# Performance work log

Hardware: AMD Instinct MI355X
Metric: run time of the kernel (lower is better)

The kernel has to match this reference:

```python
import jax, jax.numpy as jnp
import numpy as np
import math

N_EMBD = 1024
N_HEAD = 16
HEAD_DIM = N_EMBD // N_HEAD

def setup_inputs() -> dict:
    key = jax.random.key(0)
    k1, k2, k3, k4, k5 = jax.random.split(key, 5)
    s = 1.0 / math.sqrt(N_EMBD)
    x = jax.random.normal(k1, (4, 2048, N_EMBD), dtype=jnp.float32)
    W_qkv = jax.random.normal(k2, (N_EMBD, 3 * N_EMBD), dtype=jnp.float32) * s
    b_qkv = jnp.zeros((3 * N_EMBD,), dtype=jnp.float32)
    W_proj = jax.random.normal(k3, (N_EMBD, N_EMBD), dtype=jnp.float32) * s
    b_proj = jnp.zeros((N_EMBD,), dtype=jnp.float32)
    return {"x": x, "W_qkv": W_qkv, "b_qkv": b_qkv, "W_proj": W_proj, "b_proj": b_proj}

def reference(x, W_qkv, b_qkv, W_proj, b_proj):
    B, T, C = x.shape
    H, D = N_HEAD, HEAD_DIM
    qkv = x @ W_qkv + b_qkv                      # (B,T,3C)
    qkv = qkv.reshape(B, T, 3, H, D)
    q = jnp.transpose(qkv[:, :, 0], (0, 2, 1, 3))  # (B,H,T,D)
    k = jnp.transpose(qkv[:, :, 1], (0, 2, 1, 3))
    v = jnp.transpose(qkv[:, :, 2], (0, 2, 1, 3))
    scale = 1.0 / math.sqrt(D)
    att = jnp.einsum('bhtd,bhsd->bhts', q, k) * scale  # (B,H,T,T)
    causal = jnp.tril(jnp.ones((T, T), dtype=bool))
    att = jnp.where(causal[None, None], att, -jnp.inf)
    att = jax.nn.softmax(att, axis=-1)
    out = jnp.einsum('bhts,bhsd->bhtd', att, v)   # (B,H,T,D)
    out = jnp.transpose(out, (0, 2, 1, 3)).reshape(B, T, C)
    return out @ W_proj + b_proj
```

## Files before the change

kernel.cpp:

```cpp
#include <hip/hip_runtime.h>
#include <stdint.h>


typedef __attribute__((ext_vector_type(8))) __bf16 bf16x8_t;
typedef __attribute__((ext_vector_type(4))) float f32x4_t;
typedef __attribute__((ext_vector_type(16))) float f32x16_t;
typedef __attribute__((ext_vector_type(4))) unsigned short u16x4_t;
typedef __attribute__((ext_vector_type(4))) unsigned int u32x4_t;

static __device__ __forceinline__ unsigned short f2bf(float f) {
  union { float f; unsigned u; } c; c.f = f;
  unsigned r = c.u + 0x7FFFu + ((c.u >> 16) & 1u);
  return (unsigned short)(r >> 16);
}

static __device__ __forceinline__ unsigned cvt_pk_bf16(float lo, float hi) {
  unsigned r;
  asm volatile("v_cvt_pk_bf16_f32 %0, %1, %2" : "=v"(r) : "v"(lo), "v"(hi));
  return r;
}

static __device__ __forceinline__ void perm32swap(unsigned& a, unsigned& b) {
  asm volatile("v_permlane32_swap_b32 %0, %1" : "+v"(a), "+v"(b));
}

static __device__ __forceinline__ f32x16_t zero16() {
  f32x16_t v;
#pragma unroll
  for (int i = 0; i < 16; ++i) v[i] = 0.f;
  return v;
}

static __device__ __forceinline__ void gload16(const void* g, void* lds) {
  __builtin_amdgcn_global_load_lds(
      (const __attribute__((address_space(1))) unsigned int*)g,
      (__attribute__((address_space(3))) unsigned int*)(uint32_t)(uintptr_t)lds,
      16, 0, 0);
}

__global__ __launch_bounds__(256) void k_cast_bf16(const float* __restrict__ in,
                                                   unsigned short* __restrict__ out) {
  int i = blockIdx.x * 256 + threadIdx.x;
  float4 v = ((const float4*)in)[i];
  u16x4_t r = { f2bf(v.x), f2bf(v.y), f2bf(v.z), f2bf(v.w) };
  ((u16x4_t*)out)[i] = r;
}

__global__ __launch_bounds__(256) void k_transpose_cast(const float* __restrict__ W,
                                                        unsigned short* __restrict__ Wt,
                                                        int Kd, int Nd) {
  __shared__ float tile[32][33];
  int n0 = blockIdx.x * 32, k0 = blockIdx.y * 32;
  int tx = threadIdx.x, ty = threadIdx.y;
#pragma unroll
  for (int i = 0; i < 4; ++i)
    tile[ty + 8 * i][tx] = W[(size_t)(k0 + ty + 8 * i) * Nd + n0 + tx];
  __syncthreads();
#pragma unroll
  for (int i = 0; i < 4; ++i)
    Wt[(size_t)(n0 + ty + 8 * i) * Kd + k0 + tx] = f2bf(tile[tx][ty + 8 * i]);
}

static __device__ __forceinline__ void gemm_core(
    const unsigned short* __restrict__ A, const unsigned short* __restrict__ Bt,
    int Kd, int bm0, int bn0,
    unsigned short (*As)[8192], unsigned short (*Bs)[8192],
    f32x4_t acc[8][4]) {
  const int tid = threadIdx.x;
  const int lane = tid & 63;
  const int wid = tid >> 6;
  const int wm = wid >> 2, wn = wid & 3;
  const int l15 = lane & 15, lhi = (lane >> 4) & 3;
  const int r0 = tid >> 2;
  const int cd = tid & 3;
  const int NK = Kd >> 6;

  auto STAGE = [&](int kt, int h, int sl) {
#pragma unroll
    for (int j = 0; j < 2; ++j) {
      const int row = r0 + 128 * j;
      const int sc = cd ^ ((row >> 1) & 3);
      gload16(A + (size_t)(bm0 + row) * Kd + kt * 64 + h * 32 + sc * 8,
              &As[sl * 2 + h][row * 32 + cd * 8]);
    }
#pragma unroll
    for (int j = 0; j < 2; ++j) {
      const int row = r0 + 128 * j;
      const int sc = cd ^ ((row >> 1) & 3);
      gload16(Bt + (size_t)(bn0 + row) * Kd + kt * 64 + h * 32 + sc * 8,
              &Bs[sl * 2 + h][row * 32 + cd * 8]);
    }
  };

  STAGE(0, 0, 0);
  STAGE(0, 1, 0);
  for (int kt = 0; kt < NK; ++kt) {
    const int sl = kt & 1;
    const int ktn = (kt + 1 < NK) ? kt + 1 : kt;
#pragma unroll
    for (int h = 0; h < 2; ++h) {
      asm volatile("s_waitcnt vmcnt(4)" ::: "memory");
      __builtin_amdgcn_sched_barrier(0);
      __builtin_amdgcn_s_barrier();
      __builtin_amdgcn_sched_barrier(0);
      STAGE(ktn, h, sl ^ 1);
      bf16x8_t af[8], bfr[4];
#pragma unroll
      for (int m = 0; m < 8; ++m) {
        const int ar = wm * 128 + m * 16 + l15;
        af[m] = *(const bf16x8_t*)&As[sl * 2 + h][ar * 32 + ((lhi ^ ((ar >> 1) & 3)) << 3)];
      }
#pragma unroll
      for (int n = 0; n < 4; ++n) {
        const int br = wn * 64 + n * 16 + l15;
        bfr[n] = *(const bf16x8_t*)&Bs[sl * 2 + h][br * 32 + ((lhi ^ ((br >> 1) & 3)) << 3)];
      }
      __builtin_amdgcn_s_setprio(1);
#pragma unroll
      for (int m = 0; m < 8; ++m)
#pragma unroll
        for (int n = 0; n < 4; ++n)
          acc[m][n] = __builtin_amdgcn_mfma_f32_16x16x32_bf16(af[m], bfr[n], acc[m][n], 0, 0, 0);
      __builtin_amdgcn_s_setprio(0);
    }
  }
}

__global__ __launch_bounds__(512, 2) void k_gemm_qkv(
    const unsigned short* __restrict__ A, const unsigned short* __restrict__ Bt,
    const float* __restrict__ bias,
    unsigned short* __restrict__ Qo, unsigned short* __restrict__ Ko,
    unsigned short* __restrict__ Vo) {
  __shared__ alignas(16) unsigned short As[4][8192];
  __shared__ alignas(16) unsigned short Bs[4][8192];
  const int orig = blockIdx.x;
  const int swz = (orig & 7) * 48 + (orig >> 3);
  const int by = swz / 12, bx = swz % 12;
  f32x4_t acc[8][4];
  f32x4_t z = {0.f, 0.f, 0.f, 0.f};
#pragma unroll
  for (int m = 0; m < 8; ++m)
#pragma unroll
    for (int n = 0; n < 4; ++n) acc[m][n] = z;
  gemm_core(A, Bt, 1024, by * 256, bx * 256, As, Bs, acc);
  const int tid = threadIdx.x, lane = tid & 63;
  const int wid = tid >> 6, wm = wid >> 2, wn = wid & 3;
  const int l15 = lane & 15, lhi = (lane >> 4) & 3;
#pragma unroll
  for (int n = 0; n < 4; ++n) {
    int col = bx * 256 + wn * 64 + n * 16 + l15;
    int which = col >> 10;
    int h = (col >> 6) & 15;
    int d = col & 63;
    float bv = bias[col];
#pragma unroll
    for (int m = 0; m < 8; ++m)
#pragma unroll
      for (int r = 0; r < 4; ++r) {
        int row = by * 256 + wm * 128 + m * 16 + lhi * 4 + r;
        int b = row >> 11, t = row & 2047;
        float val = acc[m][n][r] + bv;
        if (which == 0)
          Qo[(size_t)((b * 16 + h) * 2048 + t) * 64 + d] = f2bf(val * 0.18033688011112042f);
        else if (which == 1)
          Ko[(size_t)((b * 16 + h) * 2048 + t) * 64 + d] = f2bf(val);
        else
          Vo[(size_t)((b * 16 + h) * 64 + d) * 2048 + t] = f2bf(val);
      }
  }
}

__global__ __launch_bounds__(512, 2) void k_gemm_proj(
    const unsigned short* __restrict__ A, const unsigned short* __restrict__ Bt,
    const float* __restrict__ bias, float* __restrict__ out) {
  __shared__ alignas(16) unsigned short As[4][8192];
  __shared__ alignas(16) unsigned short Bs[4][8192];
  const int orig = blockIdx.x;
  const int swz = (orig & 7) * 16 + (orig >> 3);
  const int by = swz >> 2, bx = swz & 3;
  f32x4_t acc[8][4];
  f32x4_t z = {0.f, 0.f, 0.f, 0.f};
#pragma unroll
  for (int m = 0; m < 8; ++m)
#pragma unroll
    for (int n = 0; n < 4; ++n) acc[m][n] = z;
  gemm_core(A, Bt, 1024, by * 256, bx * 256, As, Bs, acc);
  const int tid = threadIdx.x, lane = tid & 63;
  const int wid = tid >> 6, wm = wid >> 2, wn = wid & 3;
  const int l15 = lane & 15, lhi = (lane >> 4) & 3;
#pragma unroll
  for (int n = 0; n < 4; ++n) {
    int col = bx * 256 + wn * 64 + n * 16 + l15;
    float bv = bias[col];
#pragma unroll
    for (int m = 0; m < 8; ++m)
#pragma unroll
      for (int r = 0; r < 4; ++r) {
        int row = by * 256 + wm * 128 + m * 16 + lhi * 4 + r;
        out[(size_t)row * 1024 + col] = acc[m][n][r] + bv;
      }
  }
}

__global__ __launch_bounds__(256) void k_attn(const unsigned short* __restrict__ Q,
                                              const unsigned short* __restrict__ K,
                                              const unsigned short* __restrict__ Vt,
                                              unsigned short* __restrict__ O) {
  __shared__ alignas(16) unsigned short KT[2][4096];
  __shared__ alignas(16) unsigned short VT[2][4096];
  const int flat = blockIdx.x;
  const int bx = 15 - (flat >> 6);
  const int bh = flat & 63;
  const int tid = threadIdx.x;
  const int lane = tid & 63;
  const int w = tid >> 6;
  const int l31 = lane & 31;
  const int hi = lane >> 5;
  const int sw = l31 & 7;
  const unsigned short* Qh = Q + (size_t)bh * 2048 * 64;
  const unsigned short* Kh = K + (size_t)bh * 2048 * 64;
  const unsigned short* Vh = Vt + (size_t)bh * 64 * 2048;
  const int qrow = bx * 128 + w * 32;
  const int qg = qrow + l31;
  const int NT = 2 * bx + 2;

  bf16x8_t qf[4];
#pragma unroll
  for (int s = 0; s < 4; ++s)
    qf[s] = *(const bf16x8_t*)&Qh[(size_t)qg * 64 + s * 16 + hi * 8];

  f32x16_t ot0 = zero16(), ot1 = zero16();
  float m_r = -1e30f, l_r = 0.f;

  const int srow = tid >> 3;
  const int ssw = 8 * ((tid & 7) ^ (srow & 7));
  auto STAGE = [&](int t_, int buf_) {
#pragma unroll
    for (int i = 0; i < 2; ++i) {
      const int r_ = i * 32 + srow;
      gload16(Kh + (size_t)(t_ * 64 + r_) * 64 + ssw, &KT[buf_][i * 2048 + tid * 8]);
      gload16(Vh + (size_t)r_ * 2048 + t_ * 64 + ssw, &VT[buf_][i * 2048 + tid * 8]);
    }
  };

  STAGE(0, 0);
  __syncthreads();
  for (int t = 0; t < NT; ++t) {
    const int buf = t & 1;
    if (t + 1 < NT) STAGE(t + 1, buf ^ 1);
    if (t * 64 <= qrow + 31) {
      f32x16_t st[2];
#pragma unroll
      for (int tt = 0; tt < 2; ++tt) {
        st[tt] = zero16();
        const unsigned short* kr = &KT[buf][(tt * 32 + l31) * 64];
#pragma unroll
        for (int s = 0; s < 4; ++s) {
          bf16x8_t kf = *(const bf16x8_t*)&kr[((2 * s + hi) ^ sw) * 8];
          st[tt] = __builtin_amdgcn_mfma_f32_32x32x16_bf16(kf, qf[s], st[tt], 0, 0, 0);
        }
      }
      if (t * 64 + 63 > qrow) {
#pragma unroll
        for (int tt = 0; tt < 2; ++tt)
#pragma unroll
          for (int r = 0; r < 16; ++r) {
            int kv = t * 64 + tt * 32 + (r & 3) + 8 * (r >> 2) + 4 * hi;
            if (kv > qg) st[tt][r] = -1e30f;
          }
      }
      float mx = st[0][0];
#pragma unroll
      for (int tt = 0; tt < 2; ++tt)
#pragma unroll
        for (int r = 0; r < 16; ++r) mx = fmaxf(mx, st[tt][r]);
      mx = fmaxf(mx, __shfl_xor(mx, 32));
      float mnew = fmaxf(m_r, mx);
      float resc = __builtin_amdgcn_exp2f(m_r - mnew);
      float u = 0.f;
#pragma unroll
      for (int tt = 0; tt < 2; ++tt)
#pragma unroll
        for (int r = 0; r < 16; ++r) {
          float pv = __builtin_amdgcn_exp2f(st[tt][r] - mnew);
          st[tt][r] = pv;
          u += pv;
        }
      u += __shfl_xor(u, 32);
      l_r = l_r * resc + u;
      m_r = mnew;
      ot0 *= resc;
      ot1 *= resc;
#pragma unroll
      for (int tt = 0; tt < 2; ++tt) {
        unsigned W0 = cvt_pk_bf16(st[tt][0], st[tt][1]);
        unsigned W1 = cvt_pk_bf16(st[tt][2], st[tt][3]);
        unsigned W2 = cvt_pk_bf16(st[tt][4], st[tt][5]);
        unsigned W3 = cvt_pk_bf16(st[tt][6], st[tt][7]);
        unsigned W4 = cvt_pk_bf16(st[tt][8], st[tt][9]);
        unsigned W5 = cvt_pk_bf16(st[tt][10], st[tt][11]);
        unsigned W6 = cvt_pk_bf16(st[tt][12], st[tt][13]);
        unsigned W7 = cvt_pk_bf16(st[tt][14], st[tt][15]);
        perm32swap(W0, W2);
        perm32swap(W1, W3);
        perm32swap(W4, W6);
        perm32swap(W5, W7);
        u32x4_t fe = {W0, W1, W2, W3};
        u32x4_t fo = {W4, W5, W6, W7};
        bf16x8_t pe = __builtin_bit_cast(bf16x8_t, fe);
        bf16x8_t po = __builtin_bit_cast(bf16x8_t, fo);
        const unsigned short* vr0 = &VT[buf][l31 * 64];
        const unsigned short* vr1 = &VT[buf][(32 + l31) * 64];
        bf16x8_t ve0 = *(const bf16x8_t*)&vr0[((4 * tt + hi) ^ sw) * 8];
        bf16x8_t vo0 = *(const bf16x8_t*)&vr0[((4 * tt + 2 + hi) ^ sw) * 8];
        bf16x8_t ve1 = *(const bf16x8_t*)&vr1[((4 * tt + hi) ^ sw) * 8];
        bf16x8_t vo1 = *(const bf16x8_t*)&vr1[((4 * tt + 2 + hi) ^ sw) * 8];
        ot0 = __builtin_amdgcn_mfma_f32_32x32x16_bf16(ve0, pe, ot0, 0, 0, 0);
        ot0 = __builtin_amdgcn_mfma_f32_32x32x16_bf16(vo0, po, ot0, 0, 0, 0);
        ot1 = __builtin_amdgcn_mfma_f32_32x32x16_bf16(ve1, pe, ot1, 0, 0, 0);
        ot1 = __builtin_amdgcn_mfma_f32_32x32x16_bf16(vo1, po, ot1, 0, 0, 0);
      }
    }
    __syncthreads();
  }
  const float inv = 1.0f / l_r;
  const int b = bh >> 4, h = bh & 15;
  unsigned short* orow = O + (size_t)(b * 2048 + qg) * 1024 + h * 64;
#pragma unroll
  for (int m = 0; m < 4; ++m) {
    u16x4_t r0, r1;
#pragma unroll
    for (int j = 0; j < 4; ++j) {
      r0[j] = f2bf(ot0[4 * m + j] * inv);
      r1[j] = f2bf(ot1[4 * m + j] * inv);
    }
    *(u16x4_t*)&orow[8 * m + 4 * hi] = r0;
    *(u16x4_t*)&orow[32 + 8 * m + 4 * hi] = r1;
  }
}

extern "C" void kernel_launch(void* const* d_in, const int* in_sizes, int n_in,
                              void* d_out, int out_size, void* d_ws, size_t ws_size,
                              hipStream_t stream) {
  const float* x     = (const float*)d_in[0];
  const float* Wqkv  = (const float*)d_in[1];
  const float* bqkv  = (const float*)d_in[2];
  const float* Wproj = (const float*)d_in[3];
  const float* bproj = (const float*)d_in[4];
  float* out = (float*)d_out;

  char* ws = (char*)d_ws;
  unsigned short* xb     = (unsigned short*)(ws);
  unsigned short* wqkvT  = (unsigned short*)(ws + 16777216);
  unsigned short* wprojT = (unsigned short*)(ws + 23068672);
  unsigned short* Qb     = (unsigned short*)(ws + 25165824);
  unsigned short* Kb     = (unsigned short*)(ws + 41943040);
  unsigned short* Vb     = (unsigned short*)(ws + 58720256);
  unsigned short* Ob     = (unsigned short*)(ws + 75497472);

  k_cast_bf16<<<8192, 256, 0, stream>>>(x, xb);
  k_transpose_cast<<<dim3(96, 32), dim3(32, 8), 0, stream>>>(Wqkv, wqkvT, 1024, 3072);
  k_transpose_cast<<<dim3(32, 32), dim3(32, 8), 0, stream>>>(Wproj, wprojT, 1024, 1024);
  k_gemm_qkv<<<384, 512, 0, stream>>>(xb, wqkvT, bqkv, Qb, Kb, Vb);
  k_attn<<<1024, 256, 0, stream>>>(Qb, Kb, Vb, Ob);
  k_gemm_proj<<<128, 512, 0, stream>>>(Ob, wprojT, bproj, out);
}
```

Before: 290.9 us.

## Stage V-tile transpose through LDS and remap GEMM block-to-XCD tiling

The QKV GEMM epilogue for V columns now writes the bf16 tile into a swizzled shared buffer, then emits 16-byte coalesced stores along t into the transposed V layout, replacing scattered 2-byte strided stores. Shared memory is merged into one flat buffer so the epilogue can reuse it. Block index mapping for both GEMMs is changed so each XCD gets a 2D rectangle of tiles, aiming to improve L2 reuse of A and B panels. This adds two block barriers and an LDS round trip for the V blocks.

```diff
diff --git a/kernel.cpp b/kernel.cpp
--- a/kernel.cpp
+++ b/kernel.cpp
@@ -63,9 +63,7 @@
 
 static __device__ __forceinline__ void gemm_core(
     const unsigned short* __restrict__ A, const unsigned short* __restrict__ Bt,
-    int Kd, int bm0, int bn0,
-    unsigned short (*As)[8192], unsigned short (*Bs)[8192],
-    f32x4_t acc[8][4]) {
+    int Kd, int bm0, int bn0, unsigned short* SH, f32x4_t acc[8][4]) {
   const int tid = threadIdx.x;
   const int lane = tid & 63;
   const int wid = tid >> 6;
@@ -76,19 +74,21 @@
   const int NK = Kd >> 6;
 
   auto STAGE = [&](int kt, int h, int sl) {
+    unsigned short* Asl = SH + (sl * 2 + h) * 8192;
+    unsigned short* Bsl = SH + 32768 + (sl * 2 + h) * 8192;
 #pragma unroll
     for (int j = 0; j < 2; ++j) {
       const int row = r0 + 128 * j;
       const int sc = cd ^ ((row >> 1) & 3);
       gload16(A + (size_t)(bm0 + row) * Kd + kt * 64 + h * 32 + sc * 8,
-              &As[sl * 2 + h][row * 32 + cd * 8]);
+              &Asl[row * 32 + cd * 8]);
     }
 #pragma unroll
     for (int j = 0; j < 2; ++j) {
       const int row = r0 + 128 * j;
       const int sc = cd ^ ((row >> 1) & 3);
       gload16(Bt + (size_t)(bn0 + row) * Kd + kt * 64 + h * 32 + sc * 8,
-              &Bs[sl * 2 + h][row * 32 + cd * 8]);
+              &Bsl[row * 32 + cd * 8]);
     }
   };
 
@@ -104,16 +104,18 @@
       __builtin_amdgcn_s_barrier();
       __builtin_amdgcn_sched_barrier(0);
       STAGE(ktn, h, sl ^ 1);
+      const unsigned short* Asl = SH + (sl * 2 + h) * 8192;
+      const unsigned short* Bsl = SH + 32768 + (sl * 2 + h) * 8192;
       bf16x8_t af[8], bfr[4];
 #pragma unroll
       for (int m = 0; m < 8; ++m) {
         const int ar = wm * 128 + m * 16 + l15;
-        af[m] = *(const bf16x8_t*)&As[sl * 2 + h][ar * 32 + ((lhi ^ ((ar >> 1) & 3)) << 3)];
+        af[m] = *(const bf16x8_t*)&Asl[ar * 32 + ((lhi ^ ((ar >> 1) & 3)) << 3)];
       }
 #pragma unroll
       for (int n = 0; n < 4; ++n) {
         const int br = wn * 64 + n * 16 + l15;
-        bfr[n] = *(const bf16x8_t*)&Bs[sl * 2 + h][br * 32 + ((lhi ^ ((br >> 1) & 3)) << 3)];
+        bfr[n] = *(const bf16x8_t*)&Bsl[br * 32 + ((lhi ^ ((br >> 1) & 3)) << 3)];
       }
       __builtin_amdgcn_s_setprio(1);
 #pragma unroll
@@ -131,60 +133,88 @@
     const float* __restrict__ bias,
     unsigned short* __restrict__ Qo, unsigned short* __restrict__ Ko,
     unsigned short* __restrict__ Vo) {
-  __shared__ alignas(16) unsigned short As[4][8192];
-  __shared__ alignas(16) unsigned short Bs[4][8192];
+  __shared__ alignas(16) unsigned short SH[65536];
   const int orig = blockIdx.x;
-  const int swz = (orig & 7) * 48 + (orig >> 3);
-  const int by = swz / 12, bx = swz % 12;
+  const int xcd = orig & 7, lc = orig >> 3;
+  const int by = (xcd >> 1) * 8 + lc / 6;
+  const int bx = (xcd & 1) * 6 + lc % 6;
   f32x4_t acc[8][4];
   f32x4_t z = {0.f, 0.f, 0.f, 0.f};
 #pragma unroll
   for (int m = 0; m < 8; ++m)
 #pragma unroll
     for (int n = 0; n < 4; ++n) acc[m][n] = z;
-  gemm_core(A, Bt, 1024, by * 256, bx * 256, As, Bs, acc);
+  gemm_core(A, Bt, 1024, by * 256, bx * 256, SH, acc);
   const int tid = threadIdx.x, lane = tid & 63;
   const int wid = tid >> 6, wm = wid >> 2, wn = wid & 3;
   const int l15 = lane & 15, lhi = (lane >> 4) & 3;
-#pragma unroll
-  for (int n = 0; n < 4; ++n) {
-    int col = bx * 256 + wn * 64 + n * 16 + l15;
-    int which = col >> 10;
-    int h = (col >> 6) & 15;
-    int d = col & 63;
-    float bv = bias[col];
-#pragma unroll
-    for (int m = 0; m < 8; ++m)
-#pragma unroll
-      for (int r = 0; r < 4; ++r) {
-        int row = by * 256 + wm * 128 + m * 16 + lhi * 4 + r;
-        int b = row >> 11, t = row & 2047;
-        float val = acc[m][n][r] + bv;
-        if (which == 0)
-          Qo[(size_t)((b * 16 + h) * 2048 + t) * 64 + d] = f2bf(val * 0.18033688011112042f);
-        else if (which == 1)
-          Ko[(size_t)((b * 16 + h) * 2048 + t) * 64 + d] = f2bf(val);
-        else
-          Vo[(size_t)((b * 16 + h) * 64 + d) * 2048 + t] = f2bf(val);
-      }
+  if (bx < 8) {
+#pragma unroll
+    for (int n = 0; n < 4; ++n) {
+      int col = bx * 256 + wn * 64 + n * 16 + l15;
+      int which = col >> 10;
+      int h = (col >> 6) & 15;
+      int d = col & 63;
+      float bv = bias[col];
+      unsigned short* dst = which == 0 ? Qo : Ko;
+      float scale = which == 0 ? 0.18033688011112042f : 1.0f;
+#pragma unroll
+      for (int m = 0; m < 8; ++m)
+#pragma unroll
+        for (int r = 0; r < 4; ++r) {
+          int row = by * 256 + wm * 128 + m * 16 + lhi * 4 + r;
+          int b = row >> 11, t = row & 2047;
+          dst[(size_t)((b * 16 + h) * 2048 + t) * 64 + d] =
+              f2bf((acc[m][n][r] + bv) * scale);
+        }
+    }
+  } else {
+    __syncthreads();
+#pragma unroll
+    for (int n = 0; n < 4; ++n) {
+      const int col_l = wn * 64 + n * 16 + l15;
+      const float bv = bias[bx * 256 + col_l];
+      const int swz = (col_l & 3) << 3;
+#pragma unroll
+      for (int m = 0; m < 8; ++m) {
+        const int row0 = wm * 128 + m * 16 + lhi * 4;
+        u16x4_t pk;
+#pragma unroll
+        for (int r = 0; r < 4; ++r) pk[r] = f2bf(acc[m][n][r] + bv);
+        *(u16x4_t*)&SH[col_l * 256 + (row0 ^ swz)] = pk;
+      }
+    }
+    __syncthreads();
+#pragma unroll
+    for (int i = 0; i < 16; ++i) {
+      const int flat = i * 512 + tid;
+      const int col_l = flat >> 5;
+      const int rg8 = flat & 31;
+      bf16x8_t v = *(const bf16x8_t*)&SH[col_l * 256 + ((rg8 ^ (col_l & 3)) << 3)];
+      const int vcol = bx * 256 + col_l - 2048;
+      const int h = vcol >> 6, d = vcol & 63;
+      const int rg = by * 256 + rg8 * 8;
+      const int b = rg >> 11, t = rg & 2047;
+      *(bf16x8_t*)&Vo[((size_t)((b * 16 + h) * 64 + d)) * 2048 + t] = v;
+    }
   }
 }
 
 __global__ __launch_bounds__(512, 2) void k_gemm_proj(
     const unsigned short* __restrict__ A, const unsigned short* __restrict__ Bt,
     const float* __restrict__ bias, float* __restrict__ out) {
-  __shared__ alignas(16) unsigned short As[4][8192];
-  __shared__ alignas(16) unsigned short Bs[4][8192];
+  __shared__ alignas(16) unsigned short SH[65536];
   const int orig = blockIdx.x;
-  const int swz = (orig & 7) * 16 + (orig >> 3);
-  const int by = swz >> 2, bx = swz & 3;
+  const int xcd = orig & 7, lc = orig >> 3;
+  const int by = (xcd >> 1) * 8 + (lc >> 1);
+  const int bx = (xcd & 1) * 2 + (lc & 1);
   f32x4_t acc[8][4];
   f32x4_t z = {0.f, 0.f, 0.f, 0.f};
 #pragma unroll
   for (int m = 0; m < 8; ++m)
 #pragma unroll
     for (int n = 0; n < 4; ++n) acc[m][n] = z;
-  gemm_core(A, Bt, 1024, by * 256, bx * 256, As, Bs, acc);
+  gemm_core(A, Bt, 1024, by * 256, bx * 256, SH, acc);
   const int tid = threadIdx.x, lane = tid & 63;
   const int wid = tid >> 6, wm = wid >> 2, wn = wid & 3;
   const int l15 = lane & 15, lhi = (lane >> 4) & 3;
```

After: 257.7 us. -11.4%, faster.
